# Kernel tuning notes

Measured on AMD Instinct MI355X. Metric: run time of the kernel, lower is better.

## Reference

```python
import jax, jax.numpy as jnp
import numpy as np

N, M, D = 2048, 50000, 128


def setup_inputs() -> dict:
    key = jax.random.key(0)
    kz, kr = jax.random.split(key)
    z = jax.random.normal(kz, (N, D), dtype=jnp.float32)
    ref = jax.random.normal(kr, (M, D), dtype=jnp.float32)  # stands in for the concatenated in_dl batches
    return {"z": z, "ref": ref, "k": 10}


def reference(z, ref, k):
    # L2-normalize rows (matches z / z.norm(dim=1, keepdim=True))
    zn = z / jnp.linalg.norm(z, axis=1, keepdims=True)      # [N, D]
    rn = ref / jnp.linalg.norm(ref, axis=1, keepdims=True)  # [M, D]
    # Pairwise L2 distances via ||a||^2 + ||b||^2 - 2 a.b (same math as the
    # broadcast (rep_batch - rep_z).norm(dim=2), without the O(N*M*D) blowup).
    sq = (jnp.sum(zn * zn, axis=1)[:, None]
          + jnp.sum(rn * rn, axis=1)[None, :]
          - 2.0 * jnp.einsum('nd,md->nm', zn, rn))          # [N, M]
    dist = jnp.sqrt(jnp.maximum(sq, 1e-12))
    # Full sort along the reference axis, take the k-th smallest distance.
    return jnp.sort(dist, axis=1)[:, k]                      # [N]
```

## Files before the change

kernel.cpp:

```cpp
#include <hip/hip_runtime.h>


#define D_DIM 128
#define TQ 128
#define BR 64
#define NCH 64
#define NSUB (NCH * 16)
#define KK 11
#define CAP 256

typedef __bf16 bf16_t;
typedef bf16_t bf16x8 __attribute__((ext_vector_type(8)));
typedef float f32x4 __attribute__((ext_vector_type(4)));

__device__ __forceinline__ unsigned short f2bf(float f) {
    unsigned u = __float_as_uint(f);
    return (unsigned short)((u + 0x7fffu + ((u >> 16) & 1u)) >> 16);
}

__global__ __launch_bounds__(256) void normalize_bf16(
    const float* __restrict__ z, const float* __restrict__ ref,
    unsigned short* __restrict__ zb, unsigned short* __restrict__ rb,
    int N, int M)
{
    const int w = threadIdx.x >> 6;
    const int l = threadIdx.x & 63;
    const int row = blockIdx.x * 4 + w;
    if (row >= N + M) return;
    const float* in; unsigned short* out; int r;
    if (row < N) { in = z;   out = zb; r = row; }
    else         { in = ref; out = rb; r = row - N; }
    const float2 v = ((const float2*)in)[(size_t)r * 64 + l];
    float ss = v.x * v.x + v.y * v.y;
    #pragma unroll
    for (int off = 32; off > 0; off >>= 1) ss += __shfl_xor(ss, off);
    const float inv = rsqrtf(ss);
    ushort2 o; o.x = f2bf(v.x * inv); o.y = f2bf(v.y * inv);
    ((ushort2*)out)[(size_t)r * 64 + l] = o;
}

__device__ __forceinline__ void gld_lds16(const unsigned short* g,
                                          unsigned short* l) {
    __builtin_amdgcn_global_load_lds(
        (__attribute__((address_space(1))) void*)g,
        (__attribute__((address_space(3))) void*)l, 16, 0, 0);
}

template <int PASS>
__global__ __launch_bounds__(256, 4) void knn_pass(
    const unsigned short* __restrict__ zb, const unsigned short* __restrict__ rb,
    float* __restrict__ maxes, const float* __restrict__ T,
    int* __restrict__ cnt, float* __restrict__ surv,
    int N, int M, int chunk)
{
    __shared__ __align__(16) unsigned short Bt[2 * BR * D_DIM];

    const int nbx = (int)gridDim.x;
    const int nwg = nbx * (int)gridDim.y;
    const int bid = (int)blockIdx.x + nbx * (int)blockIdx.y;
    const int swz = (bid & 7) * (nwg >> 3) + (bid >> 3);
    const int bx = swz % nbx;
    const int by = swz / nbx;

    const int t = threadIdx.x;
    const int lane = t & 63;
    const int w = t >> 6;
    const int quad = lane >> 4;
    const int ln = lane & 15;
    const int qbase = bx * TQ;
    const int c0 = by * chunk;
    const int c1 = min(c0 + chunk, M);
    const int nt = (c1 - c0 + BR - 1) / BR;

    bf16x8 afr[2][4];
    #pragma unroll
    for (int rt = 0; rt < 2; ++rt)
        #pragma unroll
        for (int ks = 0; ks < 4; ++ks)
            afr[rt][ks] = *(const bf16x8*)
                &zb[(size_t)(qbase + w * 32 + rt * 16 + ln) * D_DIM
                    + ks * 32 + quad * 8];

    float mx[2][4];
    float tr[2][4];
    if (PASS == 1) {
        #pragma unroll
        for (int rt = 0; rt < 2; ++rt)
            #pragma unroll
            for (int r = 0; r < 4; ++r) mx[rt][r] = -3.0f;
    } else {
        #pragma unroll
        for (int rt = 0; rt < 2; ++rt)
            #pragma unroll
            for (int r = 0; r < 4; ++r)
                tr[rt][r] = T[qbase + w * 32 + rt * 16 + quad * 4 + r];
    }

    auto stage = [&](int half, int tile) {
        const int s0 = c0 + tile * BR;
        #pragma unroll
        for (int i = 0; i < 4; ++i) {
            const int r = w * 16 + i * 4 + quad;
            int g = s0 + r; if (g > M - 1) g = M - 1;
            const int sl = ln ^ (r & 15);
            gld_lds16(&rb[(size_t)g * D_DIM + sl * 8],
                      &Bt[half * (BR * D_DIM) + (w * 16 + i * 4) * D_DIM]);
        }
    };

    stage(0, 0);
    stage(1, nt > 1 ? 1 : 0);

    for (int it = 0; it < nt; ++it) {
        if (it + 1 < nt) asm volatile("s_waitcnt vmcnt(4)" ::: "memory");
        else             asm volatile("s_waitcnt vmcnt(0)" ::: "memory");
        __builtin_amdgcn_s_barrier();
        asm volatile("" ::: "memory");
        __builtin_amdgcn_sched_barrier(0);

        const int cur = it & 1;
        const int s0 = c0 + it * BR;
        const unsigned short* Bc = &Bt[cur * (BR * D_DIM)];

        f32x4 acc[2][4];
        #pragma unroll
        for (int rt = 0; rt < 2; ++rt)
            #pragma unroll
            for (int ct = 0; ct < 4; ++ct) acc[rt][ct] = (f32x4){0.f,0.f,0.f,0.f};

        __builtin_amdgcn_s_setprio(1);
        #pragma unroll
        for (int ks = 0; ks < 4; ++ks) {
            #pragma unroll
            for (int ct = 0; ct < 4; ++ct) {
                const int r = ct * 16 + ln;
                bf16x8 bfr = *(const bf16x8*)
                    &Bc[r * D_DIM + ((ks * 4 + quad) ^ ln) * 8];
                #pragma unroll
                for (int rt = 0; rt < 2; ++rt)
                    acc[rt][ct] = __builtin_amdgcn_mfma_f32_16x16x32_bf16(
                        afr[rt][ks], bfr, acc[rt][ct], 0, 0, 0);
            }
        }
        __builtin_amdgcn_s_setprio(0);

        #pragma unroll
        for (int ct = 0; ct < 4; ++ct) {
            int g = s0 + ct * 16 + ln;
            if (g < c1) {
                if (PASS == 1) {
                    #pragma unroll
                    for (int rt = 0; rt < 2; ++rt)
                        #pragma unroll
                        for (int r = 0; r < 4; ++r)
                            mx[rt][r] = fmaxf(mx[rt][r], acc[rt][ct][r]);
                } else {
                    #pragma unroll
                    for (int rt = 0; rt < 2; ++rt)
                        #pragma unroll
                        for (int r = 0; r < 4; ++r) {
                            float v = acc[rt][ct][r];
                            if (v >= tr[rt][r]) {
                                int row = qbase + w * 32 + rt * 16 + quad * 4 + r;
                                int slot = atomicAdd(&cnt[row], 1);
                                if (slot < CAP) surv[(size_t)row * CAP + slot] = v;
                            }
                        }
                }
            }
        }

        __builtin_amdgcn_sched_barrier(0);
        asm volatile("" ::: "memory");
        __builtin_amdgcn_s_barrier();
        if (it + 2 < nt) stage(cur, it + 2);
    }

    if (PASS == 1) {
        #pragma unroll
        for (int rt = 0; rt < 2; ++rt)
            #pragma unroll
            for (int r = 0; r < 4; ++r) {
                int row = qbase + w * 32 + rt * 16 + quad * 4 + r;
                maxes[(size_t)row * NSUB + by * 16 + ln] = mx[rt][r];
            }
    }
}

__device__ __forceinline__ float kth_largest_64(float* s, int kk, int t) {
    float cur = -3.0f;
    for (int it = 0; it <= kk; ++it) {
        float m = s[0];
        #pragma unroll
        for (int off = 32; off > 0; off >>= 1) m = fmaxf(m, __shfl_xor(m, off));
        cur = m;
        unsigned long long b = __ballot(s[0] == m);
        bool owner = ((int)(__ffsll(b) - 1) == t);
        #pragma unroll
        for (int j = 0; j < KK - 1; ++j) s[j] = owner ? s[j + 1] : s[j];
        if (owner) s[KK - 1] = -3.0f;
    }
    return cur;
}

__global__ __launch_bounds__(64) void knn_threshold(
    const float* __restrict__ maxes, const int* __restrict__ kp,
    float* __restrict__ T, int* __restrict__ cnt)
{
    const int row = blockIdx.x;
    const int t = threadIdx.x;
    float s[KK];
    #pragma unroll
    for (int j = 0; j < KK; ++j) s[j] = -3.0f;
    #pragma unroll
    for (int i = 0; i < NSUB / 64; ++i) {
        float v = maxes[(size_t)row * NSUB + t + 64 * i];
        #pragma unroll
        for (int j = 0; j < KK; ++j) {
            float hi = fmaxf(s[j], v), lo = fminf(s[j], v);
            s[j] = hi; v = lo;
        }
    }
    const int kk = *kp;
    float cur = kth_largest_64(s, kk, t);
    if (t == 0) { T[row] = cur; cnt[row] = 0; }
}

__global__ __launch_bounds__(64) void knn_final(
    const float* __restrict__ surv, const int* __restrict__ cnt,
    const int* __restrict__ kp, float* __restrict__ out)
{
    const int row = blockIdx.x;
    const int t = threadIdx.x;
    int c = cnt[row]; if (c > CAP) c = CAP;
    float s[KK];
    #pragma unroll
    for (int j = 0; j < KK; ++j) s[j] = -3.0f;
    #pragma unroll
    for (int i = 0; i < CAP / 64; ++i) {
        int idx = t + 64 * i;
        float v = (idx < c) ? surv[(size_t)row * CAP + idx] : -3.0f;
        #pragma unroll
        for (int j = 0; j < KK; ++j) {
            float hi = fmaxf(s[j], v), lo = fminf(s[j], v);
            s[j] = hi; v = lo;
        }
    }
    const int kk = *kp;
    float cur = kth_largest_64(s, kk, t);
    if (t == 0) out[row] = sqrtf(fmaxf(2.0f - 2.0f * cur, 1e-12f));
}

extern "C" void kernel_launch(void* const* d_in, const int* in_sizes, int n_in,
                              void* d_out, int out_size, void* d_ws, size_t ws_size,
                              hipStream_t stream) {
    const float* z   = (const float*)d_in[0];
    const float* ref = (const float*)d_in[1];
    const int*   kp  = (const int*)d_in[2];
    float* out = (float*)d_out;

    const int N = in_sizes[0] / D_DIM;
    const int M = in_sizes[1] / D_DIM;

    unsigned short* zbuf = (unsigned short*)d_ws;
    unsigned short* rbuf = zbuf + (size_t)N * D_DIM;
    float* maxes = (float*)(rbuf + (size_t)M * D_DIM);
    float* T     = maxes + (size_t)N * NSUB;
    int*   cnt   = (int*)(T + N);
    float* surv  = (float*)(cnt + N);

    normalize_bf16<<<(N + M + 3) / 4, 256, 0, stream>>>(z, ref, zbuf, rbuf, N, M);

    const int chunk = (M + NCH - 1) / NCH;
    dim3 grid(N / TQ, NCH);

    knn_pass<1><<<grid, 256, 0, stream>>>(zbuf, rbuf, maxes, nullptr,
                                          nullptr, nullptr, N, M, chunk);
    knn_threshold<<<N, 64, 0, stream>>>(maxes, kp, T, cnt);
    knn_pass<2><<<grid, 256, 0, stream>>>(zbuf, rbuf, nullptr, T,
                                          cnt, surv, N, M, chunk);
    knn_final<<<N, 64, 0, stream>>>(surv, cnt, kp, out);
}
```

Before: 158.6 us.

## Replace LDS-staged tiles with direct register B loads, wider query tiles

The distance passes drop the shared-memory double buffer with async global-to-LDS loads and barriers. Each wave now owns 64 query rows and streams 16-row reference tiles straight into registers, ping-ponging two register buffers. The query block grows to 256 rows and the reference axis is split into 128 chunks instead of 64, with a hardcoded swizzle that assumes 8 query blocks. This removes LDS traffic and block-level syncs, but each wave reloads reference rows from global/L2 with less reuse across waves, and the fixed 8-block swizzle ties the kernel to N=2048.

Result: slower. 211.9 us (+33.6%).

```diff
diff --git a/kernel.cpp b/kernel.cpp
--- a/kernel.cpp
+++ b/kernel.cpp
@@ -2,9 +2,8 @@
 
 
 #define D_DIM 128
-#define TQ 128
-#define BR 64
-#define NCH 64
+#define TQB 256
+#define NCH 128
 #define NSUB (NCH * 16)
 #define KK 11
 #define CAP 256
@@ -39,149 +38,112 @@
     ((ushort2*)out)[(size_t)r * 64 + l] = o;
 }
 
-__device__ __forceinline__ void gld_lds16(const unsigned short* g,
-                                          unsigned short* l) {
-    __builtin_amdgcn_global_load_lds(
-        (__attribute__((address_space(1))) void*)g,
-        (__attribute__((address_space(3))) void*)l, 16, 0, 0);
-}
-
 template <int PASS>
-__global__ __launch_bounds__(256, 4) void knn_pass(
+__global__ __launch_bounds__(256) void knn_pass(
     const unsigned short* __restrict__ zb, const unsigned short* __restrict__ rb,
     float* __restrict__ maxes, const float* __restrict__ T,
     int* __restrict__ cnt, float* __restrict__ surv,
     int N, int M, int chunk)
 {
-    __shared__ __align__(16) unsigned short Bt[2 * BR * D_DIM];
-
-    const int nbx = (int)gridDim.x;
-    const int nwg = nbx * (int)gridDim.y;
-    const int bid = (int)blockIdx.x + nbx * (int)blockIdx.y;
+    const int nwg = 8 * NCH;
+    const int bid = (int)blockIdx.x + 8 * (int)blockIdx.y;
     const int swz = (bid & 7) * (nwg >> 3) + (bid >> 3);
-    const int bx = swz % nbx;
-    const int by = swz / nbx;
-
-    const int t = threadIdx.x;
-    const int lane = t & 63;
-    const int w = t >> 6;
+    const int bx = swz & 7;
+    const int by = swz >> 3;
+
+    const int lane = threadIdx.x & 63;
+    const int w = threadIdx.x >> 6;
     const int quad = lane >> 4;
     const int ln = lane & 15;
-    const int qbase = bx * TQ;
+    const int rbase = bx * TQB + w * 64;
     const int c0 = by * chunk;
     const int c1 = min(c0 + chunk, M);
-    const int nt = (c1 - c0 + BR - 1) / BR;
-
-    bf16x8 afr[2][4];
-    #pragma unroll
-    for (int rt = 0; rt < 2; ++rt)
+    const int ntile = (c1 - c0 + 15) >> 4;
+
+    bf16x8 afr[4][4];
+    #pragma unroll
+    for (int rt = 0; rt < 4; ++rt)
         #pragma unroll
         for (int ks = 0; ks < 4; ++ks)
             afr[rt][ks] = *(const bf16x8*)
-                &zb[(size_t)(qbase + w * 32 + rt * 16 + ln) * D_DIM
-                    + ks * 32 + quad * 8];
-
-    float mx[2][4];
-    float tr[2][4];
+                &zb[(size_t)(rbase + rt * 16 + ln) * D_DIM + ks * 32 + quad * 8];
+
+    float mx[4][4];
+    float tr[4][4];
     if (PASS == 1) {
         #pragma unroll
-        for (int rt = 0; rt < 2; ++rt)
+        for (int rt = 0; rt < 4; ++rt)
             #pragma unroll
             for (int r = 0; r < 4; ++r) mx[rt][r] = -3.0f;
     } else {
         #pragma unroll
-        for (int rt = 0; rt < 2; ++rt)
+        for (int rt = 0; rt < 4; ++rt)
             #pragma unroll
             for (int r = 0; r < 4; ++r)
-                tr[rt][r] = T[qbase + w * 32 + rt * 16 + quad * 4 + r];
-    }
-
-    auto stage = [&](int half, int tile) {
-        const int s0 = c0 + tile * BR;
-        #pragma unroll
-        for (int i = 0; i < 4; ++i) {
-            const int r = w * 16 + i * 4 + quad;
-            int g = s0 + r; if (g > M - 1) g = M - 1;
-            const int sl = ln ^ (r & 15);
-            gld_lds16(&rb[(size_t)g * D_DIM + sl * 8],
-                      &Bt[half * (BR * D_DIM) + (w * 16 + i * 4) * D_DIM]);
+                tr[rt][r] = T[rbase + rt * 16 + quad * 4 + r];
+    }
+
+    auto loadB = [&](bf16x8* b, int tile) {
+        int g = c0 + tile * 16 + ln;
+        if (g > M - 1) g = M - 1;
+        const unsigned short* bp = &rb[(size_t)g * D_DIM + quad * 8];
+        #pragma unroll
+        for (int ks = 0; ks < 4; ++ks) b[ks] = *(const bf16x8*)(bp + ks * 32);
+    };
+
+    auto compute = [&](const bf16x8* b, int tile) {
+        f32x4 acc[4];
+        #pragma unroll
+        for (int rt = 0; rt < 4; ++rt) acc[rt] = (f32x4){0.f, 0.f, 0.f, 0.f};
+        #pragma unroll
+        for (int ks = 0; ks < 4; ++ks)
+            #pragma unroll
+            for (int rt = 0; rt < 4; ++rt)
+                acc[rt] = __builtin_amdgcn_mfma_f32_16x16x32_bf16(
+                    afr[rt][ks], b[ks], acc[rt], 0, 0, 0);
+        const int g = c0 + tile * 16 + ln;
+        if (g < c1) {
+            if (PASS == 1) {
+                #pragma unroll
+                for (int rt = 0; rt < 4; ++rt)
+                    #pragma unroll
+                    for (int r = 0; r < 4; ++r)
+                        mx[rt][r] = fmaxf(mx[rt][r], acc[rt][r]);
+            } else {
+                #pragma unroll
+                for (int rt = 0; rt < 4; ++rt)
+                    #pragma unroll
+                    for (int r = 0; r < 4; ++r) {
+                        float v = acc[rt][r];
+                        if (v >= tr[rt][r]) {
+                            int row = rbase + rt * 16 + quad * 4 + r;
+                            int slot = atomicAdd(&cnt[row], 1);
+                            if (slot < CAP) surv[(size_t)row * CAP + slot] = v;
+                        }
+                    }
+            }
         }
     };
 
-    stage(0, 0);
-    stage(1, nt > 1 ? 1 : 0);
-
-    for (int it = 0; it < nt; ++it) {
-        if (it + 1 < nt) asm volatile("s_waitcnt vmcnt(4)" ::: "memory");
-        else             asm volatile("s_waitcnt vmcnt(0)" ::: "memory");
-        __builtin_amdgcn_s_barrier();
-        asm volatile("" ::: "memory");
-        __builtin_amdgcn_sched_barrier(0);
-
-        const int cur = it & 1;
-        const int s0 = c0 + it * BR;
-        const unsigned short* Bc = &Bt[cur * (BR * D_DIM)];
-
-        f32x4 acc[2][4];
-        #pragma unroll
-        for (int rt = 0; rt < 2; ++rt)
-            #pragma unroll
-            for (int ct = 0; ct < 4; ++ct) acc[rt][ct] = (f32x4){0.f,0.f,0.f,0.f};
-
-        __builtin_amdgcn_s_setprio(1);
-        #pragma unroll
-        for (int ks = 0; ks < 4; ++ks) {
-            #pragma unroll
-            for (int ct = 0; ct < 4; ++ct) {
-                const int r = ct * 16 + ln;
-                bf16x8 bfr = *(const bf16x8*)
-                    &Bc[r * D_DIM + ((ks * 4 + quad) ^ ln) * 8];
-                #pragma unroll
-                for (int rt = 0; rt < 2; ++rt)
-                    acc[rt][ct] = __builtin_amdgcn_mfma_f32_16x16x32_bf16(
-                        afr[rt][ks], bfr, acc[rt][ct], 0, 0, 0);
-            }
-        }
-        __builtin_amdgcn_s_setprio(0);
-
-        #pragma unroll
-        for (int ct = 0; ct < 4; ++ct) {
-            int g = s0 + ct * 16 + ln;
-            if (g < c1) {
-                if (PASS == 1) {
-                    #pragma unroll
-                    for (int rt = 0; rt < 2; ++rt)
-                        #pragma unroll
-                        for (int r = 0; r < 4; ++r)
-                            mx[rt][r] = fmaxf(mx[rt][r], acc[rt][ct][r]);
-                } else {
-                    #pragma unroll
-                    for (int rt = 0; rt < 2; ++rt)
-                        #pragma unroll
-                        for (int r = 0; r < 4; ++r) {
-                            float v = acc[rt][ct][r];
-                            if (v >= tr[rt][r]) {
-                                int row = qbase + w * 32 + rt * 16 + quad * 4 + r;
-                                int slot = atomicAdd(&cnt[row], 1);
-                                if (slot < CAP) surv[(size_t)row * CAP + slot] = v;
-                            }
-                        }
-                }
-            }
-        }
-
-        __builtin_amdgcn_sched_barrier(0);
-        asm volatile("" ::: "memory");
-        __builtin_amdgcn_s_barrier();
-        if (it + 2 < nt) stage(cur, it + 2);
+    bf16x8 ba[4], bb[4];
+    loadB(ba, 0);
+    if (ntile > 1) loadB(bb, 1);
+    int tl = 0;
+    for (;;) {
+        compute(ba, tl);
+        if (tl + 2 < ntile) loadB(ba, tl + 2);
+        if (++tl >= ntile) break;
+        compute(bb, tl);
+        if (tl + 2 < ntile) loadB(bb, tl + 2);
+        if (++tl >= ntile) break;
     }
 
     if (PASS == 1) {
         #pragma unroll
-        for (int rt = 0; rt < 2; ++rt)
+        for (int rt = 0; rt < 4; ++rt)
             #pragma unroll
             for (int r = 0; r < 4; ++r) {
-                int row = qbase + w * 32 + rt * 16 + quad * 4 + r;
+                int row = rbase + rt * 16 + quad * 4 + r;
                 maxes[(size_t)row * NSUB + by * 16 + ln] = mx[rt][r];
             }
     }
@@ -272,7 +234,7 @@
     normalize_bf16<<<(N + M + 3) / 4, 256, 0, stream>>>(z, ref, zbuf, rbuf, N, M);
 
     const int chunk = (M + NCH - 1) / NCH;
-    dim3 grid(N / TQ, NCH);
+    dim3 grid(N / TQB, NCH);
 
     knn_pass<1><<<grid, 256, 0, stream>>>(zbuf, rbuf, maxes, nullptr,
                                           nullptr, nullptr, N, M, chunk);
```

## Double query rows per block and split reference into more chunks

Applied to the files above, without the earlier changes.

Each block now covers 256 query rows (64 per wave) instead of 128, so every staged reference tile feeds twice as many MFMAs and total reference traffic to LDS is halved. The reference axis is split into 96 chunks instead of 64 to keep the grid large (8x96 blocks), and the block swizzle is hardcoded for 8 query blocks. The accumulator loop is reordered per column tile to limit live accumulators, and the occupancy hint is dropped. The cost is higher register pressure (16 A fragments), possibly lower occupancy, a swizzle that assumes N=2048, and more per-chunk maxima for the threshold kernel to scan.

Measured after the change: 187.2 us. 1.18x slower.

```diff
diff --git a/kernel.cpp b/kernel.cpp
--- a/kernel.cpp
+++ b/kernel.cpp
@@ -2,9 +2,9 @@
 
 
 #define D_DIM 128
-#define TQ 128
+#define TQB 256
 #define BR 64
-#define NCH 64
+#define NCH 96
 #define NSUB (NCH * 16)
 #define KK 11
 #define CAP 256
@@ -47,7 +47,7 @@
 }
 
 template <int PASS>
-__global__ __launch_bounds__(256, 4) void knn_pass(
+__global__ __launch_bounds__(256) void knn_pass(
     const unsigned short* __restrict__ zb, const unsigned short* __restrict__ rb,
     float* __restrict__ maxes, const float* __restrict__ T,
     int* __restrict__ cnt, float* __restrict__ surv,
@@ -55,45 +55,43 @@
 {
     __shared__ __align__(16) unsigned short Bt[2 * BR * D_DIM];
 
-    const int nbx = (int)gridDim.x;
-    const int nwg = nbx * (int)gridDim.y;
-    const int bid = (int)blockIdx.x + nbx * (int)blockIdx.y;
+    const int nwg = 8 * NCH;
+    const int bid = (int)blockIdx.x + 8 * (int)blockIdx.y;
     const int swz = (bid & 7) * (nwg >> 3) + (bid >> 3);
-    const int bx = swz % nbx;
-    const int by = swz / nbx;
+    const int bx = swz & 7;
+    const int by = swz >> 3;
 
     const int t = threadIdx.x;
     const int lane = t & 63;
     const int w = t >> 6;
     const int quad = lane >> 4;
     const int ln = lane & 15;
-    const int qbase = bx * TQ;
+    const int rbase = bx * TQB + w * 64;
     const int c0 = by * chunk;
     const int c1 = min(c0 + chunk, M);
     const int nt = (c1 - c0 + BR - 1) / BR;
 
-    bf16x8 afr[2][4];
-    #pragma unroll
-    for (int rt = 0; rt < 2; ++rt)
+    bf16x8 afr[4][4];
+    #pragma unroll
+    for (int rt = 0; rt < 4; ++rt)
         #pragma unroll
         for (int ks = 0; ks < 4; ++ks)
             afr[rt][ks] = *(const bf16x8*)
-                &zb[(size_t)(qbase + w * 32 + rt * 16 + ln) * D_DIM
-                    + ks * 32 + quad * 8];
-
-    float mx[2][4];
-    float tr[2][4];
+                &zb[(size_t)(rbase + rt * 16 + ln) * D_DIM + ks * 32 + quad * 8];
+
+    float mx[4][4];
+    float tr[4][4];
     if (PASS == 1) {
         #pragma unroll
-        for (int rt = 0; rt < 2; ++rt)
+        for (int rt = 0; rt < 4; ++rt)
             #pragma unroll
             for (int r = 0; r < 4; ++r) mx[rt][r] = -3.0f;
     } else {
         #pragma unroll
-        for (int rt = 0; rt < 2; ++rt)
+        for (int rt = 0; rt < 4; ++rt)
             #pragma unroll
             for (int r = 0; r < 4; ++r)
-                tr[rt][r] = T[qbase + w * 32 + rt * 16 + quad * 4 + r];
+                tr[rt][r] = T[rbase + rt * 16 + quad * 4 + r];
     }
 
     auto stage = [&](int half, int tile) {
@@ -122,46 +120,41 @@
         const int s0 = c0 + it * BR;
         const unsigned short* Bc = &Bt[cur * (BR * D_DIM)];
 
-        f32x4 acc[2][4];
-        #pragma unroll
-        for (int rt = 0; rt < 2; ++rt)
-            #pragma unroll
-            for (int ct = 0; ct < 4; ++ct) acc[rt][ct] = (f32x4){0.f,0.f,0.f,0.f};
-
-        __builtin_amdgcn_s_setprio(1);
-        #pragma unroll
-        for (int ks = 0; ks < 4; ++ks) {
-            #pragma unroll
-            for (int ct = 0; ct < 4; ++ct) {
+        #pragma unroll
+        for (int ct = 0; ct < 4; ++ct) {
+            f32x4 acc[4];
+            #pragma unroll
+            for (int rt = 0; rt < 4; ++rt) acc[rt] = (f32x4){0.f,0.f,0.f,0.f};
+
+            __builtin_amdgcn_s_setprio(1);
+            #pragma unroll
+            for (int ks = 0; ks < 4; ++ks) {
                 const int r = ct * 16 + ln;
                 bf16x8 bfr = *(const bf16x8*)
                     &Bc[r * D_DIM + ((ks * 4 + quad) ^ ln) * 8];
                 #pragma unroll
-                for (int rt = 0; rt < 2; ++rt)
-                    acc[rt][ct] = __builtin_amdgcn_mfma_f32_16x16x32_bf16(
-                        afr[rt][ks], bfr, acc[rt][ct], 0, 0, 0);
+                for (int rt = 0; rt < 4; ++rt)
+                    acc[rt] = __builtin_amdgcn_mfma_f32_16x16x32_bf16(
+                        afr[rt][ks], bfr, acc[rt], 0, 0, 0);
             }
-        }
-        __builtin_amdgcn_s_setprio(0);
-
-        #pragma unroll
-        for (int ct = 0; ct < 4; ++ct) {
-            int g = s0 + ct * 16 + ln;
+            __builtin_amdgcn_s_setprio(0);
+
+            const int g = s0 + ct * 16 + ln;
             if (g < c1) {
                 if (PASS == 1) {
                     #pragma unroll
-                    for (int rt = 0; rt < 2; ++rt)
+                    for (int rt = 0; rt < 4; ++rt)
                         #pragma unroll
                         for (int r = 0; r < 4; ++r)
-                            mx[rt][r] = fmaxf(mx[rt][r], acc[rt][ct][r]);
+                            mx[rt][r] = fmaxf(mx[rt][r], acc[rt][r]);
                 } else {
                     #pragma unroll
-                    for (int rt = 0; rt < 2; ++rt)
+                    for (int rt = 0; rt < 4; ++rt)
                         #pragma unroll
                         for (int r = 0; r < 4; ++r) {
-                            float v = acc[rt][ct][r];
+                            float v = acc[rt][r];
                             if (v >= tr[rt][r]) {
-                                int row = qbase + w * 32 + rt * 16 + quad * 4 + r;
+                                int row = rbase + rt * 16 + quad * 4 + r;
                                 int slot = atomicAdd(&cnt[row], 1);
                                 if (slot < CAP) surv[(size_t)row * CAP + slot] = v;
                             }
@@ -178,10 +171,10 @@
 
     if (PASS == 1) {
         #pragma unroll
-        for (int rt = 0; rt < 2; ++rt)
+        for (int rt = 0; rt < 4; ++rt)
             #pragma unroll
             for (int r = 0; r < 4; ++r) {
-                int row = qbase + w * 32 + rt * 16 + quad * 4 + r;
+                int row = rbase + rt * 16 + quad * 4 + r;
                 maxes[(size_t)row * NSUB + by * 16 + ln] = mx[rt][r];
             }
     }
@@ -272,7 +265,7 @@
     normalize_bf16<<<(N + M + 3) / 4, 256, 0, stream>>>(z, ref, zbuf, rbuf, N, M);
 
     const int chunk = (M + NCH - 1) / NCH;
-    dim3 grid(N / TQ, NCH);
+    dim3 grid(N / TQB, NCH);
 
     knn_pass<1><<<grid, 256, 0, stream>>>(zbuf, rbuf, maxes, nullptr,
                                           nullptr, nullptr, N, M, chunk);
```
